# Kernel optimization log

Measured on AMD Instinct MI355X. Metric: run time of the kernel, lower is better.

## Reference

```python
import jax, jax.numpy as jnp
import numpy as np

B_, T_, IDIM, D, H, FF, L, MAXLEN = 8, 512, 1799, 256, 4, 2048, 16, 1000
DK = D // H


def _ln(x, g, b, eps=1e-12):
    m = jnp.mean(x, axis=-1, keepdims=True)
    v = jnp.mean((x - m) ** 2, axis=-1, keepdims=True)
    return (x - m) * jax.lax.rsqrt(v + eps) * g + b


def setup_inputs() -> dict:
    key = jax.random.key(0)
    ks = jax.random.split(key, 16)
    s = 0.02
    n = lambda k, shape: jax.random.normal(k, shape, jnp.float32) * s
    return {
        'xs': jax.random.normal(ks[0], (B_, T_, IDIM), jnp.float32),
        'masks': jnp.ones((B_, 1, T_), jnp.int32),
        'emb_w': n(ks[1], (D, IDIM)), 'emb_b': jnp.zeros((D,), jnp.float32),
        'emb_g': jnp.ones((D,), jnp.float32), 'emb_beta': jnp.zeros((D,), jnp.float32),
        'pe_k': n(ks[2], (2 * MAXLEN, DK)),
        'Wq': n(ks[3], (L, D, D)), 'bq': jnp.zeros((L, D), jnp.float32),
        'Wk': n(ks[4], (L, D, D)), 'bk': jnp.zeros((L, D), jnp.float32),
        'Wv': n(ks[5], (L, D, D)), 'bv': jnp.zeros((L, D), jnp.float32),
        'Wo': n(ks[6], (L, D, D)), 'bo': jnp.zeros((L, D), jnp.float32),
        'ln1_g': jnp.ones((L, D), jnp.float32), 'ln1_b': jnp.zeros((L, D), jnp.float32),
        'ln2_g': jnp.ones((L, D), jnp.float32), 'ln2_b': jnp.zeros((L, D), jnp.float32),
        'lnk_g': jnp.ones((L, DK), jnp.float32), 'lnk_b': jnp.zeros((L, DK), jnp.float32),
        'W1': n(ks[7], (L, FF, D)), 'b1': jnp.zeros((L, FF), jnp.float32),
        'W2': n(ks[8], (L, D, FF)), 'b2': jnp.zeros((L, D), jnp.float32),
        'after_g': jnp.ones((D,), jnp.float32), 'after_b': jnp.zeros((D,), jnp.float32),
    }


def reference(xs, masks, emb_w, emb_b, emb_g, emb_beta, pe_k, Wq, bq, Wk, bk, Wv, bv, Wo, bo,
              ln1_g, ln1_b, ln2_g, ln2_b, lnk_g, lnk_b, W1, b1, W2, b2, after_g, after_b):
    # embed: Linear -> LayerNorm -> (Dropout=id) -> ReLU
    x = jax.nn.relu(_ln(xs @ emb_w.T + emb_b, emb_g, emb_beta))  # [B,T,D]
    # relative position table gather: pos_k [T,T,DK]
    pos = jnp.arange(T_)
    rel = jnp.clip(pos[:, None] - pos[None, :], -MAXLEN, MAXLEN - 1) + MAXLEN
    pos_k = pe_k[rel]
    neg = (masks == 0)[:, None, :, :]  # [B,1,1,T]
    minval = jnp.finfo(x.dtype).min
    scale = 1.0 / np.sqrt(DK).astype(np.float32)

    def block(x, p):
        y = _ln(x, p['ln1_g'], p['ln1_b'])
        pk = _ln(pos_k, p['lnk_g'], p['lnk_b'])  # norm_k applied per layer
        proj = lambda W, b: (y @ W.T + b).reshape(B_, T_, H, DK).transpose(0, 2, 1, 3)
        q = proj(p['Wq'], p['bq'])  # [B,H,T,DK]
        k = proj(p['Wk'], p['bk'])
        v = proj(p['Wv'], p['bv'])
        A = jnp.einsum('bhtd,bhsd->bhts', q, k)
        Bt = jnp.einsum('bhtd,tsd->bhts', q, pk)  # rel-pos bias term
        scores = jnp.where(neg, minval, (A + Bt) * scale)
        attn = jnp.where(neg, 0.0, jax.nn.softmax(scores, axis=-1))
        o = jnp.einsum('bhts,bhsd->bhtd', attn, v)
        o = o.transpose(0, 2, 1, 3).reshape(B_, T_, D)
        x = x + o @ p['Wo'].T + p['bo']
        y2 = _ln(x, p['ln2_g'], p['ln2_b'])
        ff = jax.nn.relu(y2 @ p['W1'].T + p['b1']) @ p['W2'].T + p['b2']
        return x + ff, None

    params = {'Wq': Wq, 'bq': bq, 'Wk': Wk, 'bk': bk, 'Wv': Wv, 'bv': bv, 'Wo': Wo, 'bo': bo,
              'ln1_g': ln1_g, 'ln1_b': ln1_b, 'ln2_g': ln2_g, 'ln2_b': ln2_b,
              'lnk_g': lnk_g, 'lnk_b': lnk_b, 'W1': W1, 'b1': b1, 'W2': W2, 'b2': b2}
    x, _ = jax.lax.scan(block, x, params)
    return _ln(x, after_g, after_b)
```

## Files before the change

kernel.cpp:

```cpp
#include <hip/hip_runtime.h>
#include <cstdint>


typedef __bf16 bf16_t;
typedef bf16_t bf16x4 __attribute__((ext_vector_type(4)));
typedef bf16_t bf16x8 __attribute__((ext_vector_type(8)));
typedef float  f32x4  __attribute__((ext_vector_type(4)));

#define B_    8
#define T_    512
#define IDIM  1799
#define KPAD  1824
#define D_    256
#define H_    4
#define DK    64
#define FF_   2048
#define L_    16
#define NROW  4096
#define PKROWS 2000
#define NBH   32
#define NSA   4

__device__ __forceinline__ f32x4 mfma16(bf16x8 a, bf16x8 b, f32x4 c) {
  return __builtin_amdgcn_mfma_f32_16x16x32_bf16(a, b, c, 0, 0, 0);
}

__device__ __forceinline__ void async_cp16(const void* g, void* l) {
  __builtin_amdgcn_global_load_lds(
      (__attribute__((address_space(1))) void*)(g),
      (__attribute__((address_space(3))) void*)(l), 16, 0, 0);
}

__global__ __launch_bounds__(256) void cvt_f32_bf16(const float* __restrict__ s,
                                                    bf16_t* __restrict__ d, int n) {
  int i = blockIdx.x * 256 + threadIdx.x;
  int stride = gridDim.x * 256;
  for (; i < n; i += stride) d[i] = (bf16_t)s[i];
}

__global__ __launch_bounds__(256) void cvt_pad_row(const float* __restrict__ s,
                                                   bf16_t* __restrict__ d,
                                                   int ksrc, int kdst) {
  const int r = blockIdx.x;
  const float* sr = s + (size_t)r * ksrc;
  bf16_t* dr = d + (size_t)r * kdst;
  for (int k = threadIdx.x; k < kdst; k += 256)
    dr[k] = (k < ksrc) ? (bf16_t)sr[k] : (bf16_t)0.f;
}

__global__ __launch_bounds__(256) void pack_qkvw(const float* __restrict__ wq,
                                                 const float* __restrict__ wk,
                                                 const float* __restrict__ wv,
                                                 bf16_t* __restrict__ dst) {
  const int per_l = 768 * 256;
  int i = blockIdx.x * 256 + threadIdx.x;
  int stride = gridDim.x * 256;
  for (; i < L_ * per_l; i += stride) {
    int l = i / per_l, r = i - l * per_l;
    int n = r >> 8, c = r & 255;
    int sel = n >> 8, nn = n & 255;
    const float* w = (sel == 0) ? wq : (sel == 1) ? wk : wv;
    dst[i] = (bf16_t)w[((size_t)l * 256 + nn) * 256 + c];
  }
}

__global__ __launch_bounds__(256) void pack_qkvb(const float* __restrict__ bq,
                                                 const float* __restrict__ bk,
                                                 const float* __restrict__ bv,
                                                 float* __restrict__ dst) {
  int i = blockIdx.x * 256 + threadIdx.x;
  if (i >= L_ * 768) return;
  int l = i / 768, n = i - l * 768;
  int sel = n >> 8, nn = n & 255;
  const float* b = (sel == 0) ? bq : (sel == 1) ? bk : bv;
  dst[i] = b[l * 256 + nn];
}

__global__ __launch_bounds__(256) void pkn_ln(const float* __restrict__ pe_k,
                                              const float* __restrict__ lnk_g,
                                              const float* __restrict__ lnk_b,
                                              bf16_t* __restrict__ out) {
  const int idx = blockIdx.x * 4 + (threadIdx.x >> 6);
  if (idx >= L_ * PKROWS) return;
  const int lane = threadIdx.x & 63;
  const int l = idx / PKROWS, r = idx - l * PKROWS;
  float v = pe_k[(size_t)r * DK + lane];
  float s = v;
#pragma unroll
  for (int o = 32; o; o >>= 1) s += __shfl_xor(s, o);
  const float mean = s * (1.f / DK);
  const float dx = v - mean;
  float q = dx * dx;
#pragma unroll
  for (int o = 32; o; o >>= 1) q += __shfl_xor(q, o);
  const float rs = rsqrtf(q * (1.f / DK) + 1e-12f);
  out[((size_t)l * PKROWS + r) * DK + lane] =
      (bf16_t)(dx * rs * lnk_g[l * DK + lane] + lnk_b[l * DK + lane]);
}

template <bool BF16OUT, bool RELU>
__global__ __launch_bounds__(256) void ln_rows(const float* __restrict__ src,
                                               const float* __restrict__ g,
                                               const float* __restrict__ b,
                                               void* __restrict__ dst) {
  const int row = blockIdx.x * 4 + (threadIdx.x >> 6);
  const int lane = threadIdx.x & 63;
  const float4 v = ((const float4*)(src + (size_t)row * D_))[lane];
  float s = v.x + v.y + v.z + v.w;
#pragma unroll
  for (int o = 32; o; o >>= 1) s += __shfl_xor(s, o);
  const float mean = s * (1.f / D_);
  const float d0 = v.x - mean, d1 = v.y - mean, d2 = v.z - mean, d3 = v.w - mean;
  float q = d0 * d0 + d1 * d1 + d2 * d2 + d3 * d3;
#pragma unroll
  for (int o = 32; o; o >>= 1) q += __shfl_xor(q, o);
  const float rs = rsqrtf(q * (1.f / D_) + 1e-12f);
  const float4 gg = ((const float4*)g)[lane];
  const float4 bb = ((const float4*)b)[lane];
  float o0 = d0 * rs * gg.x + bb.x;
  float o1 = d1 * rs * gg.y + bb.y;
  float o2 = d2 * rs * gg.z + bb.z;
  float o3 = d3 * rs * gg.w + bb.w;
  if (RELU) {
    o0 = fmaxf(o0, 0.f); o1 = fmaxf(o1, 0.f);
    o2 = fmaxf(o2, 0.f); o3 = fmaxf(o3, 0.f);
  }
  if (BF16OUT) {
    bf16x4 o4 = {(bf16_t)o0, (bf16_t)o1, (bf16_t)o2, (bf16_t)o3};
    ((bf16x4*)((bf16_t*)dst + (size_t)row * D_))[lane] = o4;
  } else {
    ((float4*)((float*)dst + (size_t)row * D_))[lane] = make_float4(o0, o1, o2, o3);
  }
}

template <int NS, bool WRITE_Y>
__global__ __launch_bounds__(256) void add_combine_ln(
    const float* __restrict__ parts, const float* __restrict__ bias,
    float* __restrict__ x, const float* __restrict__ g,
    const float* __restrict__ b, bf16_t* __restrict__ y) {
  const int row = blockIdx.x * 4 + (threadIdx.x >> 6);
  const int lane = threadIdx.x & 63;
  const size_t idx = (size_t)row * 64 + lane;
  float4 v = ((const float4*)x)[idx];
#pragma unroll
  for (int p = 0; p < NS; ++p) {
    float4 pv = ((const float4*)parts)[(size_t)p * NROW * 64 + idx];
    v.x += pv.x; v.y += pv.y; v.z += pv.z; v.w += pv.w;
  }
  const float4 bi = ((const float4*)bias)[lane];
  v.x += bi.x; v.y += bi.y; v.z += bi.z; v.w += bi.w;
  ((float4*)x)[idx] = v;
  if (WRITE_Y) {
    float s = v.x + v.y + v.z + v.w;
#pragma unroll
    for (int o = 32; o; o >>= 1) s += __shfl_xor(s, o);
    const float mean = s * (1.f / D_);
    const float d0 = v.x - mean, d1 = v.y - mean, d2 = v.z - mean, d3 = v.w - mean;
    float q = d0 * d0 + d1 * d1 + d2 * d2 + d3 * d3;
#pragma unroll
    for (int o = 32; o; o >>= 1) q += __shfl_xor(q, o);
    const float rs = rsqrtf(q * (1.f / D_) + 1e-12f);
    const float4 gg = ((const float4*)g)[lane];
    const float4 bb = ((const float4*)b)[lane];
    bf16x4 o4 = {(bf16_t)(d0 * rs * gg.x + bb.x), (bf16_t)(d1 * rs * gg.y + bb.y),
                 (bf16_t)(d2 * rs * gg.z + bb.z), (bf16_t)(d3 * rs * gg.w + bb.w)};
    ((bf16x4*)y)[idx] = o4;
  }
}

__global__ __launch_bounds__(256) void embed_combine(
    const float* __restrict__ parts, const float* __restrict__ bias,
    const float* __restrict__ g, const float* __restrict__ b,
    float* __restrict__ x) {
  const int row = blockIdx.x * 4 + (threadIdx.x >> 6);
  const int lane = threadIdx.x & 63;
  const size_t idx = (size_t)row * 64 + lane;
  float4 v = ((const float4*)parts)[idx];
  float4 p1 = ((const float4*)parts)[(size_t)NROW * 64 + idx];
  const float4 bi = ((const float4*)bias)[lane];
  v.x += p1.x + bi.x; v.y += p1.y + bi.y; v.z += p1.z + bi.z; v.w += p1.w + bi.w;
  float s = v.x + v.y + v.z + v.w;
#pragma unroll
  for (int o = 32; o; o >>= 1) s += __shfl_xor(s, o);
  const float mean = s * (1.f / D_);
  const float d0 = v.x - mean, d1 = v.y - mean, d2 = v.z - mean, d3 = v.w - mean;
  float q = d0 * d0 + d1 * d1 + d2 * d2 + d3 * d3;
#pragma unroll
  for (int o = 32; o; o >>= 1) q += __shfl_xor(q, o);
  const float rs = rsqrtf(q * (1.f / D_) + 1e-12f);
  const float4 gg = ((const float4*)g)[lane];
  const float4 bb = ((const float4*)b)[lane];
  ((float4*)x)[idx] = make_float4(
      fmaxf(d0 * rs * gg.x + bb.x, 0.f), fmaxf(d1 * rs * gg.y + bb.y, 0.f),
      fmaxf(d2 * rs * gg.z + bb.z, 0.f), fmaxf(d3 * rs * gg.w + bb.w, 0.f));
}

template <int BM, int BN, int EP>
__global__ __launch_bounds__(256, 2) void gemm_bf16(
    const bf16_t* __restrict__ A, int lda, const bf16_t* __restrict__ B, int ldb,
    const float* __restrict__ bias, void* __restrict__ Cout, int ldc,
    const float* __restrict__ resid, int K, size_t zstride) {
  constexpr int HM = BM / 2, HN = BN / 2;
  constexpr int FM = HM / 16, FN = HN / 16;
  constexpr int CA = (BM * 4) / 256, CB = (BN * 4) / 256;
  __shared__ bf16_t lsA[BM * 32];
  __shared__ bf16_t lsB[BN * 32];
  const int tid = threadIdx.x;
  const int w = tid >> 6, lane = tid & 63;
  const int wm = w >> 1, wn = w & 1;
  const int lanelo = lane & 15, quad = lane >> 4;
  const int wbase = tid & ~63;
  const int m0 = blockIdx.x * BM, n0 = blockIdx.y * BN;
  const int ktiles = K >> 5;
  const int tpz = (ktiles + gridDim.z - 1) / gridDim.z;
  const int kb = blockIdx.z * tpz * 32;
  const int ke = min(K, kb + tpz * 32);
  f32x4 acc[FM][FN] = {};

  for (int kt = kb; kt < ke; kt += 32) {
    __syncthreads();
#pragma unroll
    for (int rr = 0; rr < CA; ++rr) {
      int chunk = rr * 256 + tid;
      int r = chunk >> 2, qs = chunk & 3;
      int qg = qs ^ ((r >> 1) & 3);
      async_cp16(A + (size_t)(m0 + r) * lda + kt + qg * 8,
                 lsA + (size_t)(rr * 256 + wbase) * 8);
    }
#pragma unroll
    for (int rr = 0; rr < CB; ++rr) {
      int chunk = rr * 256 + tid;
      int r = chunk >> 2, qs = chunk & 3;
      int qg = qs ^ ((r >> 1) & 3);
      async_cp16(B + (size_t)(n0 + r) * ldb + kt + qg * 8,
                 lsB + (size_t)(rr * 256 + wbase) * 8);
    }
    __syncthreads();
    bf16x8 af[FM], bfv[FN];
#pragma unroll
    for (int i = 0; i < FM; ++i) {
      int r = wm * HM + i * 16 + lanelo;
      af[i] = *(const bf16x8*)(lsA + (size_t)(r * 4 + (quad ^ ((r >> 1) & 3))) * 8);
    }
#pragma unroll
    for (int j = 0; j < FN; ++j) {
      int r = wn * HN + j * 16 + lanelo;
      bfv[j] = *(const bf16x8*)(lsB + (size_t)(r * 4 + (quad ^ ((r >> 1) & 3))) * 8);
    }
#pragma unroll
    for (int i = 0; i < FM; ++i)
#pragma unroll
      for (int j = 0; j < FN; ++j) acc[i][j] = mfma16(af[i], bfv[j], acc[i][j]);
  }

#pragma unroll
  for (int i = 0; i < FM; ++i) {
#pragma unroll
    for (int j = 0; j < FN; ++j) {
#pragma unroll
      for (int reg = 0; reg < 4; ++reg) {
        const int m = m0 + wm * HM + i * 16 + quad * 4 + reg;
        const int n = n0 + wn * HN + j * 16 + lanelo;
        const size_t idx = (size_t)m * ldc + n;
        if constexpr (EP == 4) {
          ((float*)Cout + (size_t)blockIdx.z * zstride)[idx] = acc[i][j][reg];
        } else {
          float v = acc[i][j][reg] + bias[n];
          if constexpr (EP == 0) {
            ((float*)Cout)[idx] = v;
          } else if constexpr (EP == 1) {
            ((bf16_t*)Cout)[idx] = (bf16_t)v;
          } else if constexpr (EP == 2) {
            ((bf16_t*)Cout)[idx] = (bf16_t)fmaxf(v, 0.f);
          } else {
            ((float*)Cout)[idx] = v + resid[idx];
          }
        }
      }
    }
  }
}

__global__ __launch_bounds__(256, 3) void attn_part(
    const bf16_t* __restrict__ qkv, const bf16_t* __restrict__ pkn,
    const int* __restrict__ masks, float* __restrict__ Opart,
    float* __restrict__ mpart, float* __restrict__ lpart) {
  __shared__ bf16_t ls_q[64 * 72];
  __shared__ bf16_t ls_kr[128 * 66];
  __shared__ bf16_t ls_vt[64 * 72];
  __shared__ bf16_t ls_pk[128 * 72];
  bf16_t* const ls_k = ls_kr;
  bf16_t* const ls_r = ls_kr;
  bf16_t* const ls_p = ls_pk;

  const int tid = threadIdx.x, w = tid >> 6, lane = tid & 63;
  const int lanelo = lane & 15, quad = lane >> 4;
  const int t0 = blockIdx.x * 64;
  const int bh = blockIdx.y, bb = bh >> 2, h = bh & 3;
  const int z = blockIdx.z;
  const size_t rowbase = (size_t)bb * T_;

  for (int c = tid; c < 64 * 8; c += 256) {
    int r = c >> 3, c8 = (c & 7) * 8;
    *(bf16x8*)&ls_q[r * 72 + c8] =
        *(const bf16x8*)(qkv + (rowbase + t0 + r) * 768 + h * 64 + c8);
  }
  __syncthreads();
  bf16x8 qf[2];
  qf[0] = *(const bf16x8*)&ls_q[(w * 16 + lanelo) * 72 + quad * 8];
  qf[1] = *(const bf16x8*)&ls_q[(w * 16 + lanelo) * 72 + 32 + quad * 8];

  f32x4 o_acc[4] = {};
  float m_run[4], l_run[4];
#pragma unroll
  for (int i = 0; i < 4; ++i) { m_run[i] = -__builtin_inff(); l_run[i] = 0.f; }

  for (int st = 2 * z; st < 2 * z + 2; ++st) {
    const int s0 = st * 64;
    __syncthreads();
    for (int c = tid; c < 64 * 8; c += 256) {
      int r = c >> 3, c8 = (c & 7) * 8;
      *(bf16x8*)&ls_k[r * 72 + c8] =
          *(const bf16x8*)(qkv + (rowbase + s0 + r) * 768 + 256 + h * 64 + c8);
    }
    for (int c = tid; c < 64 * 8; c += 256) {
      int r = c & 63, d0 = (c >> 6) * 8;
      bf16x8 vv = *(const bf16x8*)(qkv + (rowbase + s0 + r) * 768 + 512 + h * 64 + d0);
#pragma unroll
      for (int i = 0; i < 8; ++i) ls_vt[(d0 + i) * 72 + r] = vv[i];
    }
    {
      const int base = t0 - s0 + 937;
      for (int c = tid; c < 128 * 8; c += 256) {
        int r = c >> 3, c8 = (c & 7) * 8;
        *(bf16x8*)&ls_pk[r * 72 + c8] =
            *(const bf16x8*)(pkn + (size_t)(base + r) * DK + c8);
      }
    }
    __syncthreads();

    f32x4 sacc[4] = {};
#pragma unroll
    for (int kk = 0; kk < 2; ++kk)
#pragma unroll
      for (int nf = 0; nf < 4; ++nf) {
        bf16x8 bk = *(const bf16x8*)&ls_k[(nf * 16 + lanelo) * 72 + kk * 32 + quad * 8];
        sacc[nf] = mfma16(qf[kk], bk, sacc[nf]);
      }
    f32x4 racc[8] = {};
#pragma unroll
    for (int kk = 0; kk < 2; ++kk)
#pragma unroll
      for (int jf = 0; jf < 8; ++jf) {
        bf16x8 bfr = *(const bf16x8*)&ls_pk[(jf * 16 + lanelo) * 72 + kk * 32 + quad * 8];
        racc[jf] = mfma16(qf[kk], bfr, racc[jf]);
      }
    __syncthreads();

#pragma unroll
    for (int jf = 0; jf < 8; ++jf)
#pragma unroll
      for (int reg = 0; reg < 4; ++reg)
        ls_r[(jf * 16 + lanelo) * 66 + w * 16 + quad * 4 + reg] =
            (bf16_t)racc[jf][reg];

    float sv[4][4], pmask[4];
#pragma unroll
    for (int nf = 0; nf < 4; ++nf) {
      const int scol = nf * 16 + lanelo;
      const int mk = masks[bb * T_ + s0 + scol];
      pmask[nf] = mk ? 1.f : 0.f;
#pragma unroll
      for (int reg = 0; reg < 4; ++reg) {
        const int trow = w * 16 + quad * 4 + reg;
        const float bt = (float)ls_r[(trow - scol + 63) * 66 + trow];
        const float val = (sacc[nf][reg] + bt) * 0.125f;
        sv[nf][reg] = mk ? val : -3.4028235e38f;
      }
    }
    float alpha[4];
#pragma unroll
    for (int reg = 0; reg < 4; ++reg) {
      float bm = fmaxf(fmaxf(sv[0][reg], sv[1][reg]), fmaxf(sv[2][reg], sv[3][reg]));
#pragma unroll
      for (int o = 1; o < 16; o <<= 1) bm = fmaxf(bm, __shfl_xor(bm, o));
      const float mn = fmaxf(m_run[reg], bm);
      alpha[reg] = __expf(m_run[reg] - mn);
      m_run[reg] = mn;
      float rsum = 0.f;
#pragma unroll
      for (int nf = 0; nf < 4; ++nf) {
        float p = __expf(sv[nf][reg] - mn) * pmask[nf];
        sv[nf][reg] = p;
        rsum += p;
      }
#pragma unroll
      for (int o = 1; o < 16; o <<= 1) rsum += __shfl_xor(rsum, o);
      l_run[reg] = l_run[reg] * alpha[reg] + rsum;
    }
#pragma unroll
    for (int nf = 0; nf < 4; ++nf)
#pragma unroll
      for (int reg = 0; reg < 4; ++reg) {
        o_acc[nf][reg] *= alpha[reg];
        ls_p[(w * 16 + quad * 4 + reg) * 72 + nf * 16 + lanelo] = (bf16_t)sv[nf][reg];
      }
#pragma unroll
    for (int kk = 0; kk < 2; ++kk) {
      bf16x8 ap = *(const bf16x8*)&ls_p[(w * 16 + lanelo) * 72 + kk * 32 + quad * 8];
#pragma unroll
      for (int nf = 0; nf < 4; ++nf) {
        bf16x8 bv = *(const bf16x8*)&ls_vt[(nf * 16 + lanelo) * 72 + kk * 32 + quad * 8];
        o_acc[nf] = mfma16(ap, bv, o_acc[nf]);
      }
    }
  }

#pragma unroll
  for (int reg = 0; reg < 4; ++reg) {
    const int trow = w * 16 + quad * 4 + reg;
    const size_t prow = ((size_t)z * NBH + bh) * T_ + t0 + trow;
#pragma unroll
    for (int nf = 0; nf < 4; ++nf)
      Opart[prow * 64 + nf * 16 + lanelo] = o_acc[nf][reg];
    if (lanelo == 0) { mpart[prow] = m_run[reg]; lpart[prow] = l_run[reg]; }
  }
}

__global__ __launch_bounds__(256) void attn_combine(
    const float* __restrict__ Opart, const float* __restrict__ mpart,
    const float* __restrict__ lpart, bf16_t* __restrict__ ao) {
  const int hr = blockIdx.x * 4 + (threadIdx.x >> 6);
  const int lane = threadIdx.x & 63;
  const int bh = hr >> 9, t = hr & 511;
  float mp[NSA], lp[NSA];
  float m = -__builtin_inff();
#pragma unroll
  for (int p = 0; p < NSA; ++p) {
    const size_t prow = ((size_t)p * NBH + bh) * T_ + t;
    mp[p] = mpart[prow]; lp[p] = lpart[prow];
    m = fmaxf(m, mp[p]);
  }
  float denom = 0.f, o = 0.f;
#pragma unroll
  for (int p = 0; p < NSA; ++p) {
    if (lp[p] > 0.f) {
      const float wp = __expf(mp[p] - m);
      denom += lp[p] * wp;
      o += Opart[(((size_t)p * NBH + bh) * T_ + t) * 64 + lane] * wp;
    }
  }
  const float res = (denom > 0.f) ? o / denom : 0.f;
  const int bb = bh >> 2, hh = bh & 3;
  ao[((size_t)bb * T_ + t) * D_ + hh * 64 + lane] = (bf16_t)res;
}

extern "C" void kernel_launch(void* const* d_in, const int* in_sizes, int n_in,
                              void* d_out, int out_size, void* d_ws, size_t ws_size,
                              hipStream_t stream) {
  const float* xs       = (const float*)d_in[0];
  const int*   masks    = (const int*)d_in[1];
  const float* emb_w    = (const float*)d_in[2];
  const float* emb_b    = (const float*)d_in[3];
  const float* emb_g    = (const float*)d_in[4];
  const float* emb_beta = (const float*)d_in[5];
  const float* pe_k     = (const float*)d_in[6];
  const float* Wq       = (const float*)d_in[7];
  const float* bq       = (const float*)d_in[8];
  const float* Wk       = (const float*)d_in[9];
  const float* bk       = (const float*)d_in[10];
  const float* Wv       = (const float*)d_in[11];
  const float* bv       = (const float*)d_in[12];
  const float* Wo       = (const float*)d_in[13];
  const float* bo       = (const float*)d_in[14];
  const float* ln1_g    = (const float*)d_in[15];
  const float* ln1_b    = (const float*)d_in[16];
  const float* ln2_g    = (const float*)d_in[17];
  const float* ln2_b    = (const float*)d_in[18];
  const float* lnk_g    = (const float*)d_in[19];
  const float* lnk_b    = (const float*)d_in[20];
  const float* W1       = (const float*)d_in[21];
  const float* b1       = (const float*)d_in[22];
  const float* W2       = (const float*)d_in[23];
  const float* b2       = (const float*)d_in[24];
  const float* after_g  = (const float*)d_in[25];
  const float* after_b  = (const float*)d_in[26];

  char* ws = (char*)d_ws;
  size_t off = 0;
  auto take = [&](size_t bytes) -> void* {
    void* p = ws + off;
    off += (bytes + 255) & ~(size_t)255;
    return p;
  };
  bf16_t* ewb  = (bf16_t*)take((size_t)D_ * KPAD * 2);
  bf16_t* wcat = (bf16_t*)take((size_t)L_ * 768 * D_ * 2);
  float*  bcat = (float*) take((size_t)L_ * 768 * 4);
  bf16_t* wob  = (bf16_t*)take((size_t)L_ * D_ * D_ * 2);
  bf16_t* w1b  = (bf16_t*)take((size_t)L_ * FF_ * D_ * 2);
  bf16_t* w2b  = (bf16_t*)take((size_t)L_ * D_ * FF_ * 2);
  bf16_t* pknb = (bf16_t*)take((size_t)L_ * PKROWS * DK * 2);
  float*  x    = (float*) take((size_t)NROW * D_ * 4);
  bf16_t* y    = (bf16_t*)take((size_t)NROW * D_ * 2);
  bf16_t* qkv  = (bf16_t*)take((size_t)NROW * 768 * 2);
  bf16_t* ao   = (bf16_t*)take((size_t)NROW * D_ * 2);
  bf16_t* hbuf = (bf16_t*)take((size_t)NROW * FF_ * 2);
  float*  Opart = (float*)take((size_t)NSA * NBH * T_ * 64 * 4);
  float*  mpart = (float*)take((size_t)NSA * NBH * T_ * 4);
  float*  lpart = (float*)take((size_t)NSA * NBH * T_ * 4);
  float*  gpart = Opart;
  bf16_t* xsb  = hbuf;
  const size_t ZS = (size_t)NROW * D_;

  cvt_pad_row<<<NROW, 256, 0, stream>>>(xs, xsb, IDIM, KPAD);
  cvt_pad_row<<<D_, 256, 0, stream>>>(emb_w, ewb, IDIM, KPAD);
  pack_qkvw<<<2048, 256, 0, stream>>>(Wq, Wk, Wv, wcat);
  pack_qkvb<<<48, 256, 0, stream>>>(bq, bk, bv, bcat);
  cvt_f32_bf16<<<1024, 256, 0, stream>>>(Wo, wob, L_ * D_ * D_);
  cvt_f32_bf16<<<2048, 256, 0, stream>>>(W1, w1b, L_ * FF_ * D_);
  cvt_f32_bf16<<<2048, 256, 0, stream>>>(W2, w2b, L_ * D_ * FF_);
  pkn_ln<<<(L_ * PKROWS) / 4, 256, 0, stream>>>(pe_k, lnk_g, lnk_b, pknb);

  gemm_bf16<64, 64, 4><<<dim3(NROW / 64, D_ / 64, 2), 256, 0, stream>>>(
      xsb, KPAD, ewb, KPAD, nullptr, gpart, D_, nullptr, KPAD, ZS);
  embed_combine<<<NROW / 4, 256, 0, stream>>>(gpart, emb_b, emb_g, emb_beta, x);
  ln_rows<true, false><<<NROW / 4, 256, 0, stream>>>(x, ln1_g, ln1_b, y);

  for (int l = 0; l < L_; ++l) {
    gemm_bf16<64, 64, 1><<<dim3(NROW / 64, 768 / 64), 256, 0, stream>>>(
        y, D_, wcat + (size_t)l * 768 * D_, D_, bcat + l * 768, qkv, 768, nullptr,
        D_, 0);
    attn_part<<<dim3(T_ / 64, NBH, NSA), 256, 0, stream>>>(
        qkv, pknb + (size_t)l * PKROWS * DK, masks, Opart, mpart, lpart);
    attn_combine<<<NBH * T_ / 4, 256, 0, stream>>>(Opart, mpart, lpart, ao);
    gemm_bf16<64, 64, 4><<<dim3(NROW / 64, D_ / 64, 2), 256, 0, stream>>>(
        ao, D_, wob + (size_t)l * D_ * D_, D_, nullptr, gpart, D_, nullptr, D_, ZS);
    add_combine_ln<2, true><<<NROW / 4, 256, 0, stream>>>(
        gpart, bo + l * D_, x, ln2_g + l * D_, ln2_b + l * D_, y);
    gemm_bf16<128, 128, 2><<<dim3(NROW / 128, FF_ / 128), 256, 0, stream>>>(
        y, D_, w1b + (size_t)l * FF_ * D_, D_, b1 + l * FF_, hbuf, FF_, nullptr,
        D_, 0);
    gemm_bf16<64, 64, 4><<<dim3(NROW / 64, D_ / 64, 2), 256, 0, stream>>>(
        hbuf, FF_, w2b + (size_t)l * D_ * FF_, FF_, nullptr, gpart, D_, nullptr,
        FF_, ZS);
    if (l < L_ - 1) {
      add_combine_ln<2, true><<<NROW / 4, 256, 0, stream>>>(
          gpart, b2 + l * D_, x, ln1_g + (l + 1) * D_, ln1_b + (l + 1) * D_, y);
    } else {
      add_combine_ln<2, false><<<NROW / 4, 256, 0, stream>>>(
          gpart, b2 + l * D_, x, nullptr, nullptr, nullptr);
    }
  }
  ln_rows<false, false><<<NROW / 4, 256, 0, stream>>>(x, after_g, after_b,
                                                      (float*)d_out);
}
```

Measured before the change: 1.545 ms.

## Deepen GEMM K-tile, split rel-pos bias into own GEMM, bf16 attention partials

The GEMM now uses a 64-wide K tile with an 8-way XOR swizzle, so each barrier pair covers twice the MFMA work. KPAD grows to a multiple of 64 to match, and occupancy hints are tuned per instantiation. The relative-position bias is computed once per (query tile, head) by a new bt_gemm kernel and written as a full bf16 T×T matrix, which attn_part reads back instead of redoing the banded pk product for every key chunk. Attention partial outputs are stored as bf16 and Q/K loads become async swizzled copies, at the cost of extra global traffic for the bias matrix and lower precision in the partials.

New measurement: 1.436 ms. -7.1%, faster.

```diff
diff --git a/kernel.cpp b/kernel.cpp
--- a/kernel.cpp
+++ b/kernel.cpp
@@ -10,7 +10,7 @@
 #define B_    8
 #define T_    512
 #define IDIM  1799
-#define KPAD  1824
+#define KPAD  1856
 #define D_    256
 #define H_    4
 #define DK    64
@@ -195,62 +195,69 @@
       fmaxf(d2 * rs * gg.z + bb.z, 0.f), fmaxf(d3 * rs * gg.w + bb.w, 0.f));
 }
 
-template <int BM, int BN, int EP>
-__global__ __launch_bounds__(256, 2) void gemm_bf16(
+template <int BM, int BN, int EP, int MINW>
+__global__ __launch_bounds__(256, MINW) void gemm_bf16(
     const bf16_t* __restrict__ A, int lda, const bf16_t* __restrict__ B, int ldb,
     const float* __restrict__ bias, void* __restrict__ Cout, int ldc,
     const float* __restrict__ resid, int K, size_t zstride) {
   constexpr int HM = BM / 2, HN = BN / 2;
   constexpr int FM = HM / 16, FN = HN / 16;
-  constexpr int CA = (BM * 4) / 256, CB = (BN * 4) / 256;
-  __shared__ bf16_t lsA[BM * 32];
-  __shared__ bf16_t lsB[BN * 32];
+  constexpr int CA = (BM * 8) / 256, CB = (BN * 8) / 256;
+  __shared__ bf16_t lsA[BM * 64];
+  __shared__ bf16_t lsB[BN * 64];
   const int tid = threadIdx.x;
   const int w = tid >> 6, lane = tid & 63;
   const int wm = w >> 1, wn = w & 1;
   const int lanelo = lane & 15, quad = lane >> 4;
   const int wbase = tid & ~63;
   const int m0 = blockIdx.x * BM, n0 = blockIdx.y * BN;
-  const int ktiles = K >> 5;
+  const int ktiles = K >> 6;
   const int tpz = (ktiles + gridDim.z - 1) / gridDim.z;
-  const int kb = blockIdx.z * tpz * 32;
-  const int ke = min(K, kb + tpz * 32);
+  const int kb = blockIdx.z * tpz * 64;
+  const int ke = min(K, kb + tpz * 64);
   f32x4 acc[FM][FN] = {};
 
-  for (int kt = kb; kt < ke; kt += 32) {
+  for (int kt = kb; kt < ke; kt += 64) {
     __syncthreads();
 #pragma unroll
     for (int rr = 0; rr < CA; ++rr) {
       int chunk = rr * 256 + tid;
-      int r = chunk >> 2, qs = chunk & 3;
-      int qg = qs ^ ((r >> 1) & 3);
-      async_cp16(A + (size_t)(m0 + r) * lda + kt + qg * 8,
+      int r = chunk >> 3, c8 = chunk & 7;
+      int lg = c8 ^ (r & 7);
+      async_cp16(A + (size_t)(m0 + r) * lda + kt + lg * 8,
                  lsA + (size_t)(rr * 256 + wbase) * 8);
     }
 #pragma unroll
     for (int rr = 0; rr < CB; ++rr) {
       int chunk = rr * 256 + tid;
-      int r = chunk >> 2, qs = chunk & 3;
-      int qg = qs ^ ((r >> 1) & 3);
-      async_cp16(B + (size_t)(n0 + r) * ldb + kt + qg * 8,
+      int r = chunk >> 3, c8 = chunk & 7;
+      int lg = c8 ^ (r & 7);
+      async_cp16(B + (size_t)(n0 + r) * ldb + kt + lg * 8,
                  lsB + (size_t)(rr * 256 + wbase) * 8);
     }
     __syncthreads();
-    bf16x8 af[FM], bfv[FN];
+    bf16x8 af[FM][2], bfv[FN][2];
 #pragma unroll
     for (int i = 0; i < FM; ++i) {
       int r = wm * HM + i * 16 + lanelo;
-      af[i] = *(const bf16x8*)(lsA + (size_t)(r * 4 + (quad ^ ((r >> 1) & 3))) * 8);
+#pragma unroll
+      for (int kk = 0; kk < 2; ++kk)
+        af[i][kk] = *(const bf16x8*)(lsA + (size_t)(r * 8 + ((kk * 4 + quad) ^ (r & 7))) * 8);
     }
 #pragma unroll
     for (int j = 0; j < FN; ++j) {
       int r = wn * HN + j * 16 + lanelo;
-      bfv[j] = *(const bf16x8*)(lsB + (size_t)(r * 4 + (quad ^ ((r >> 1) & 3))) * 8);
-    }
-#pragma unroll
-    for (int i = 0; i < FM; ++i)
-#pragma unroll
-      for (int j = 0; j < FN; ++j) acc[i][j] = mfma16(af[i], bfv[j], acc[i][j]);
+#pragma unroll
+      for (int kk = 0; kk < 2; ++kk)
+        bfv[j][kk] = *(const bf16x8*)(lsB + (size_t)(r * 8 + ((kk * 4 + quad) ^ (r & 7))) * 8);
+    }
+#pragma unroll
+    for (int kk = 0; kk < 2; ++kk)
+#pragma unroll
+      for (int i = 0; i < FM; ++i)
+#pragma unroll
+        for (int j = 0; j < FN; ++j)
+          acc[i][j] = mfma16(af[i][kk], bfv[j][kk], acc[i][j]);
   }
 
 #pragma unroll
@@ -281,34 +288,106 @@
   }
 }
 
-__global__ __launch_bounds__(256, 3) void attn_part(
+__global__ __launch_bounds__(256, 3) void bt_gemm(
     const bf16_t* __restrict__ qkv, const bf16_t* __restrict__ pkn,
-    const int* __restrict__ masks, float* __restrict__ Opart,
+    bf16_t* __restrict__ Bt) {
+  __shared__ bf16_t ls_q[64 * 64];
+  __shared__ bf16_t ls_j[192 * 64];
+  const int tid = threadIdx.x, w = tid >> 6, lane = tid & 63;
+  const int wm = w >> 1, wn = w & 1;
+  const int lanelo = lane & 15, quad = lane >> 4;
+  const int wbase = tid & ~63;
+  const int t0 = blockIdx.x * 64;
+  const int bh = blockIdx.y, bb = bh >> 2, h = bh & 3;
+  const size_t rowbase = (size_t)bb * T_;
+  const int relbase = t0 + 489;
+
+#pragma unroll
+  for (int rr = 0; rr < 2; ++rr) {
+    int chunk = rr * 256 + tid;
+    int r = chunk >> 3, c8 = chunk & 7;
+    int lg = c8 ^ (r & 7);
+    async_cp16(qkv + (rowbase + t0 + r) * 768 + h * 64 + lg * 8,
+               ls_q + (size_t)(rr * 256 + wbase) * 8);
+  }
+  __syncthreads();
+  bf16x8 qf[2][2];
+#pragma unroll
+  for (int i = 0; i < 2; ++i) {
+    int r = wm * 32 + i * 16 + lanelo;
+#pragma unroll
+    for (int kk = 0; kk < 2; ++kk)
+      qf[i][kk] = *(const bf16x8*)(ls_q + (size_t)(r * 8 + ((kk * 4 + quad) ^ (r & 7))) * 8);
+  }
+
+  for (int jc = 0; jc < 3; ++jc) {
+    if (jc) __syncthreads();
+#pragma unroll
+    for (int rr = 0; rr < 6; ++rr) {
+      int chunk = rr * 256 + tid;
+      int r = chunk >> 3, c8 = chunk & 7;
+      int lg = c8 ^ (r & 7);
+      async_cp16(pkn + (size_t)(relbase + jc * 192 + r) * DK + lg * 8,
+                 ls_j + (size_t)(rr * 256 + wbase) * 8);
+    }
+    __syncthreads();
+    f32x4 racc[2][6] = {};
+#pragma unroll
+    for (int kk = 0; kk < 2; ++kk)
+#pragma unroll
+      for (int nf = 0; nf < 6; ++nf) {
+        int r = wn * 96 + nf * 16 + lanelo;
+        bf16x8 bj = *(const bf16x8*)(ls_j + (size_t)(r * 8 + ((kk * 4 + quad) ^ (r & 7))) * 8);
+#pragma unroll
+        for (int i = 0; i < 2; ++i) racc[i][nf] = mfma16(qf[i][kk], bj, racc[i][nf]);
+      }
+#pragma unroll
+    for (int i = 0; i < 2; ++i)
+#pragma unroll
+      for (int nf = 0; nf < 6; ++nf)
+#pragma unroll
+        for (int reg = 0; reg < 4; ++reg) {
+          const int tl = wm * 32 + i * 16 + quad * 4 + reg;
+          const int jj = jc * 192 + wn * 96 + nf * 16 + lanelo;
+          const int s = tl + 511 - jj;
+          if (s >= 0 && s < T_)
+            Bt[(((size_t)bh * T_ + t0 + tl) << 9) + s] = (bf16_t)racc[i][nf][reg];
+        }
+  }
+}
+
+__global__ __launch_bounds__(256, 4) void attn_part(
+    const bf16_t* __restrict__ qkv, const bf16_t* __restrict__ Bt,
+    const int* __restrict__ masks, bf16_t* __restrict__ Opart,
     float* __restrict__ mpart, float* __restrict__ lpart) {
-  __shared__ bf16_t ls_q[64 * 72];
-  __shared__ bf16_t ls_kr[128 * 66];
+  __shared__ bf16_t ls_q[64 * 64];
+  __shared__ bf16_t ls_k[64 * 64];
   __shared__ bf16_t ls_vt[64 * 72];
-  __shared__ bf16_t ls_pk[128 * 72];
-  bf16_t* const ls_k = ls_kr;
-  bf16_t* const ls_r = ls_kr;
-  bf16_t* const ls_p = ls_pk;
+  __shared__ bf16_t ls_p[64 * 72];
 
   const int tid = threadIdx.x, w = tid >> 6, lane = tid & 63;
   const int lanelo = lane & 15, quad = lane >> 4;
+  const int wbase = tid & ~63;
   const int t0 = blockIdx.x * 64;
   const int bh = blockIdx.y, bb = bh >> 2, h = bh & 3;
   const int z = blockIdx.z;
   const size_t rowbase = (size_t)bb * T_;
 
-  for (int c = tid; c < 64 * 8; c += 256) {
-    int r = c >> 3, c8 = (c & 7) * 8;
-    *(bf16x8*)&ls_q[r * 72 + c8] =
-        *(const bf16x8*)(qkv + (rowbase + t0 + r) * 768 + h * 64 + c8);
+#pragma unroll
+  for (int rr = 0; rr < 2; ++rr) {
+    int chunk = rr * 256 + tid;
+    int r = chunk >> 3, c8 = chunk & 7;
+    int lg = c8 ^ (r & 7);
+    async_cp16(qkv + (rowbase + t0 + r) * 768 + h * 64 + lg * 8,
+               ls_q + (size_t)(rr * 256 + wbase) * 8);
   }
   __syncthreads();
   bf16x8 qf[2];
-  qf[0] = *(const bf16x8*)&ls_q[(w * 16 + lanelo) * 72 + quad * 8];
-  qf[1] = *(const bf16x8*)&ls_q[(w * 16 + lanelo) * 72 + 32 + quad * 8];
+#pragma unroll
+  for (int kk = 0; kk < 2; ++kk) {
+    int r = w * 16 + lanelo;
+    qf[kk] = *(const bf16x8*)(ls_q + (size_t)(r * 8 + ((kk * 4 + quad) ^ (r & 7))) * 8);
+  }
 
   f32x4 o_acc[4] = {};
   float m_run[4], l_run[4];
@@ -318,66 +397,51 @@
   for (int st = 2 * z; st < 2 * z + 2; ++st) {
     const int s0 = st * 64;
     __syncthreads();
-    for (int c = tid; c < 64 * 8; c += 256) {
-      int r = c >> 3, c8 = (c & 7) * 8;
-      *(bf16x8*)&ls_k[r * 72 + c8] =
-          *(const bf16x8*)(qkv + (rowbase + s0 + r) * 768 + 256 + h * 64 + c8);
-    }
+#pragma unroll
+    for (int rr = 0; rr < 2; ++rr) {
+      int chunk = rr * 256 + tid;
+      int r = chunk >> 3, c8 = chunk & 7;
+      int lg = c8 ^ (r & 7);
+      async_cp16(qkv + (rowbase + s0 + r) * 768 + 256 + h * 64 + lg * 8,
+                 ls_k + (size_t)(rr * 256 + wbase) * 8);
+    }
+#pragma unroll
     for (int c = tid; c < 64 * 8; c += 256) {
       int r = c & 63, d0 = (c >> 6) * 8;
       bf16x8 vv = *(const bf16x8*)(qkv + (rowbase + s0 + r) * 768 + 512 + h * 64 + d0);
 #pragma unroll
       for (int i = 0; i < 8; ++i) ls_vt[(d0 + i) * 72 + r] = vv[i];
     }
-    {
-      const int base = t0 - s0 + 937;
-      for (int c = tid; c < 128 * 8; c += 256) {
-        int r = c >> 3, c8 = (c & 7) * 8;
-        *(bf16x8*)&ls_pk[r * 72 + c8] =
-            *(const bf16x8*)(pkn + (size_t)(base + r) * DK + c8);
+    __syncthreads();
+
+    float btv[4][4];
+    int mk[4];
+#pragma unroll
+    for (int nf = 0; nf < 4; ++nf) {
+      const int scol = nf * 16 + lanelo;
+      mk[nf] = masks[bb * T_ + s0 + scol];
+#pragma unroll
+      for (int reg = 0; reg < 4; ++reg) {
+        const int trow = w * 16 + quad * 4 + reg;
+        btv[nf][reg] = (float)Bt[(((size_t)bh * T_ + t0 + trow) << 9) + s0 + scol];
       }
     }
-    __syncthreads();
-
     f32x4 sacc[4] = {};
 #pragma unroll
     for (int kk = 0; kk < 2; ++kk)
 #pragma unroll
       for (int nf = 0; nf < 4; ++nf) {
-        bf16x8 bk = *(const bf16x8*)&ls_k[(nf * 16 + lanelo) * 72 + kk * 32 + quad * 8];
+        int r = nf * 16 + lanelo;
+        bf16x8 bk = *(const bf16x8*)(ls_k + (size_t)(r * 8 + ((kk * 4 + quad) ^ (r & 7))) * 8);
         sacc[nf] = mfma16(qf[kk], bk, sacc[nf]);
       }
-    f32x4 racc[8] = {};
-#pragma unroll
-    for (int kk = 0; kk < 2; ++kk)
-#pragma unroll
-      for (int jf = 0; jf < 8; ++jf) {
-        bf16x8 bfr = *(const bf16x8*)&ls_pk[(jf * 16 + lanelo) * 72 + kk * 32 + quad * 8];
-        racc[jf] = mfma16(qf[kk], bfr, racc[jf]);
-      }
-    __syncthreads();
-
-#pragma unroll
-    for (int jf = 0; jf < 8; ++jf)
+    float sv[4][4];
+#pragma unroll
+    for (int nf = 0; nf < 4; ++nf)
 #pragma unroll
       for (int reg = 0; reg < 4; ++reg)
-        ls_r[(jf * 16 + lanelo) * 66 + w * 16 + quad * 4 + reg] =
-            (bf16_t)racc[jf][reg];
-
-    float sv[4][4], pmask[4];
-#pragma unroll
-    for (int nf = 0; nf < 4; ++nf) {
-      const int scol = nf * 16 + lanelo;
-      const int mk = masks[bb * T_ + s0 + scol];
-      pmask[nf] = mk ? 1.f : 0.f;
-#pragma unroll
-      for (int reg = 0; reg < 4; ++reg) {
-        const int trow = w * 16 + quad * 4 + reg;
-        const float bt = (float)ls_r[(trow - scol + 63) * 66 + trow];
-        const float val = (sacc[nf][reg] + bt) * 0.125f;
-        sv[nf][reg] = mk ? val : -3.4028235e38f;
-      }
-    }
+        sv[nf][reg] = mk[nf] ? (sacc[nf][reg] + btv[nf][reg]) * 0.125f
+                             : -3.4028235e38f;
     float alpha[4];
 #pragma unroll
     for (int reg = 0; reg < 4; ++reg) {
@@ -390,7 +454,7 @@
       float rsum = 0.f;
 #pragma unroll
       for (int nf = 0; nf < 4; ++nf) {
-        float p = __expf(sv[nf][reg] - mn) * pmask[nf];
+        float p = __expf(sv[nf][reg] - mn) * (mk[nf] ? 1.f : 0.f);
         sv[nf][reg] = p;
         rsum += p;
       }
@@ -422,13 +486,13 @@
     const size_t prow = ((size_t)z * NBH + bh) * T_ + t0 + trow;
 #pragma unroll
     for (int nf = 0; nf < 4; ++nf)
-      Opart[prow * 64 + nf * 16 + lanelo] = o_acc[nf][reg];
+      Opart[prow * 64 + nf * 16 + lanelo] = (bf16_t)o_acc[nf][reg];
     if (lanelo == 0) { mpart[prow] = m_run[reg]; lpart[prow] = l_run[reg]; }
   }
 }
 
 __global__ __launch_bounds__(256) void attn_combine(
-    const float* __restrict__ Opart, const float* __restrict__ mpart,
+    const bf16_t* __restrict__ Opart, const float* __restrict__ mpart,
     const float* __restrict__ lpart, bf16_t* __restrict__ ao) {
   const int hr = blockIdx.x * 4 + (threadIdx.x >> 6);
   const int lane = threadIdx.x & 63;
@@ -447,7 +511,7 @@
     if (lp[p] > 0.f) {
       const float wp = __expf(mp[p] - m);
       denom += lp[p] * wp;
-      o += Opart[(((size_t)p * NBH + bh) * T_ + t) * 64 + lane] * wp;
+      o += (float)Opart[(((size_t)p * NBH + bh) * T_ + t) * 64 + lane] * wp;
     }
   }
   const float res = (denom > 0.f) ? o / denom : 0.f;
@@ -505,10 +569,11 @@
   bf16_t* qkv  = (bf16_t*)take((size_t)NROW * 768 * 2);
   bf16_t* ao   = (bf16_t*)take((size_t)NROW * D_ * 2);
   bf16_t* hbuf = (bf16_t*)take((size_t)NROW * FF_ * 2);
-  float*  Opart = (float*)take((size_t)NSA * NBH * T_ * 64 * 4);
+  bf16_t* Btb  = (bf16_t*)take((size_t)NBH * T_ * T_ * 2);
+  bf16_t* Opart = (bf16_t*)take((size_t)NSA * NBH * T_ * 64 * 2);
   float*  mpart = (float*)take((size_t)NSA * NBH * T_ * 4);
   float*  lpart = (float*)take((size_t)NSA * NBH * T_ * 4);
-  float*  gpart = Opart;
+  float*  gpart = (float*)take((size_t)2 * NROW * D_ * 4);
   bf16_t* xsb  = hbuf;
   const size_t ZS = (size_t)NROW * D_;
 
@@ -521,26 +586,28 @@
   cvt_f32_bf16<<<2048, 256, 0, stream>>>(W2, w2b, L_ * D_ * FF_);
   pkn_ln<<<(L_ * PKROWS) / 4, 256, 0, stream>>>(pe_k, lnk_g, lnk_b, pknb);
 
-  gemm_bf16<64, 64, 4><<<dim3(NROW / 64, D_ / 64, 2), 256, 0, stream>>>(
+  gemm_bf16<64, 64, 4, 3><<<dim3(NROW / 64, D_ / 64, 2), 256, 0, stream>>>(
       xsb, KPAD, ewb, KPAD, nullptr, gpart, D_, nullptr, KPAD, ZS);
   embed_combine<<<NROW / 4, 256, 0, stream>>>(gpart, emb_b, emb_g, emb_beta, x);
   ln_rows<true, false><<<NROW / 4, 256, 0, stream>>>(x, ln1_g, ln1_b, y);
 
   for (int l = 0; l < L_; ++l) {
-    gemm_bf16<64, 64, 1><<<dim3(NROW / 64, 768 / 64), 256, 0, stream>>>(
+    gemm_bf16<64, 64, 1, 3><<<dim3(NROW / 64, 768 / 64), 256, 0, stream>>>(
         y, D_, wcat + (size_t)l * 768 * D_, D_, bcat + l * 768, qkv, 768, nullptr,
         D_, 0);
+    bt_gemm<<<dim3(T_ / 64, NBH), 256, 0, stream>>>(
+        qkv, pknb + (size_t)l * PKROWS * DK, Btb);
     attn_part<<<dim3(T_ / 64, NBH, NSA), 256, 0, stream>>>(
-        qkv, pknb + (size_t)l * PKROWS * DK, masks, Opart, mpart, lpart);
+        qkv, Btb, masks, Opart, mpart, lpart);
     attn_combine<<<NBH * T_ / 4, 256, 0, stream>>>(Opart, mpart, lpart, ao);
-    gemm_bf16<64, 64, 4><<<dim3(NROW / 64, D_ / 64, 2), 256, 0, stream>>>(
+    gemm_bf16<64, 64, 4, 3><<<dim3(NROW / 64, D_ / 64, 2), 256, 0, stream>>>(
         ao, D_, wob + (size_t)l * D_ * D_, D_, nullptr, gpart, D_, nullptr, D_, ZS);
     add_combine_ln<2, true><<<NROW / 4, 256, 0, stream>>>(
         gpart, bo + l * D_, x, ln2_g + l * D_, ln2_b + l * D_, y);
-    gemm_bf16<128, 128, 2><<<dim3(NROW / 128, FF_ / 128), 256, 0, stream>>>(
+    gemm_bf16<128, 128, 2, 2><<<dim3(NROW / 128, FF_ / 128), 256, 0, stream>>>(
         y, D_, w1b + (size_t)l * FF_ * D_, D_, b1 + l * FF_, hbuf, FF_, nullptr,
         D_, 0);
-    gemm_bf16<64, 64, 4><<<dim3(NROW / 64, D_ / 64, 2), 256, 0, stream>>>(
+    gemm_bf16<64, 64, 4, 3><<<dim3(NROW / 64, D_ / 64, 2), 256, 0, stream>>>(
         hbuf, FF_, w2b + (size_t)l * D_ * FF_, FF_, nullptr, gpart, D_, nullptr,
         FF_, ZS);
     if (l < L_ - 1) {
```
